# Kernel optimization log

Hardware: AMD Instinct MI355X
Metric: run time of the kernel (lower is better)

The kernel has to match this reference:

```python
import jax, jax.numpy as jnp
import numpy as np

NUM_HEADS = 12
AGENT_NUM = 49

def setup_inputs() -> dict:
    key = jax.random.key(0)
    ks = jax.random.split(key, 5)
    B, N, C = 32, 1176, 768
    x = jax.random.normal(ks[0], (B, N, C), dtype=jnp.float32)
    qkv_w = jax.random.normal(ks[1], (3 * C, C), dtype=jnp.float32) * 0.02
    qkv_b = jax.random.normal(ks[2], (3 * C,), dtype=jnp.float32) * 0.02
    proj_w = jax.random.normal(ks[3], (C, C), dtype=jnp.float32) * 0.02
    proj_b = jax.random.normal(ks[4], (C,), dtype=jnp.float32) * 0.02
    return {"x": x, "qkv_w": qkv_w, "qkv_b": qkv_b, "proj_w": proj_w,
            "proj_b": proj_b, "t_h": 14, "t_w": 14, "s_h": 28, "s_w": 28}

def _softmax_clamped(a):
    # original: float32 clamp to finfo min/max, then softmax(dim=-1)
    fi = jnp.finfo(jnp.float32)
    a = jnp.clip(a.astype(jnp.float32), fi.min, fi.max)
    return jax.nn.softmax(a, axis=-1)

def reference(x, qkv_w, qkv_b, proj_w, proj_b, t_h, t_w, s_h, s_w):
    B, N, C = x.shape
    H = NUM_HEADS
    hd = C // H
    scale = hd ** -0.5
    n_mt = 2 * t_h * t_w
    n_s = s_h * s_w

    qkv = (x @ qkv_w.T + qkv_b).reshape(B, N, 3, H, hd).transpose(2, 0, 3, 1, 4)
    q, k, v = qkv[0], qkv[1], qkv[2]  # [B,H,N,hd]

    q_mt, q_s = q[:, :, :n_mt], q[:, :, n_mt:]
    k_mt = k[:, :, :n_mt]
    v_mt = v[:, :, :n_mt]

    # stage 1: template/memory self-attention
    attn = _softmax_clamped(jnp.einsum('bhqd,bhkd->bhqk', q_mt, k_mt) * scale)
    x_mt = jnp.einsum('bhqk,bhkd->bhqd', attn, v_mt).transpose(0, 2, 1, 3).reshape(B, n_mt, C)

    # agent tokens: pool q_s (replicates original layout-scrambling reshape)
    p = int(AGENT_NUM ** 0.5)  # 7
    agent = q_s.reshape(B, s_h, s_w, C).transpose(0, 3, 1, 2)  # [B,C,s_h,s_w]
    agent = agent.reshape(B, C, p, s_h // p, p, s_w // p).mean(axis=(3, 5))  # exact AdaptiveAvgPool2d(7,7)
    agent = agent.reshape(B, C, AGENT_NUM).transpose(0, 2, 1)  # [B,agent_num,C]
    agent = agent.reshape(B, AGENT_NUM, H, hd).transpose(0, 2, 1, 3)  # [B,H,agent_num,hd]

    # stage 2: agent attends to all keys
    agent_attn = _softmax_clamped(jnp.einsum('bhad,bhkd->bhak', agent * scale, k))
    agent_v = jnp.einsum('bhak,bhkd->bhad', agent_attn, v)  # [B,H,agent_num,hd]

    # stage 3: search queries attend to agent tokens
    q_attn = _softmax_clamped(jnp.einsum('bhqd,bhad->bhqa', q_s * scale, agent))
    x_s = jnp.einsum('bhqa,bhad->bhqd', q_attn, agent_v).transpose(0, 2, 1, 3).reshape(B, n_s, C)

    out = jnp.concatenate([x_mt, x_s], axis=1)
    out = out @ proj_w.T + proj_b
    return out
```

## Files before the change

kernel.cpp:

```cpp
#include <hip/hip_runtime.h>

typedef __attribute__((ext_vector_type(8))) short short8;
typedef __attribute__((ext_vector_type(4))) short short4v;
typedef __attribute__((ext_vector_type(4))) float f32x4;
typedef unsigned short u16;

#define B_    32
#define N_    1176
#define C_    768
#define H_    12
#define HD_   64
#define NMT_  392
#define AG_   49
#define NEGBIG_ (-1.0e4f)

__device__ __forceinline__ u16 f2bf(float f) {
  unsigned u = __float_as_uint(f);
  unsigned r = (u + 0x7fffu + ((u >> 16) & 1u)) >> 16;
  return (u16)r;
}
__device__ __forceinline__ float bf2f(u16 s) {
  return __uint_as_float(((unsigned)s) << 16);
}

__device__ __forceinline__ int xcd_swz(int g, int nwg) {
  const int q = nwg >> 3, r = nwg & 7;
  const int xcd = g & 7, off = g >> 3;
  return (xcd < r ? xcd * (q + 1) : r * (q + 1) + (xcd - r) * q) + off;
}

__global__ __launch_bounds__(256) void split_all(
    const float* __restrict__ x, u16* __restrict__ xbf, int n4x,
    const float* __restrict__ qw, u16* __restrict__ qwh, int n4q,
    const float* __restrict__ pw, u16* __restrict__ pwh,
    u16* __restrict__ pwl, int n4p) {
  const int bid = blockIdx.x;
  const float* in;
  u16 *hi, *lo = nullptr;
  int n4, i0, nblk;
  if (bid < 2048) {
    in = x; hi = xbf; n4 = n4x; i0 = bid; nblk = 2048;
  } else if (bid < 3072) {
    in = qw; hi = qwh; n4 = n4q; i0 = bid - 2048; nblk = 1024;
  } else {
    in = pw; hi = pwh; lo = pwl; n4 = n4p; i0 = bid - 3072; nblk = 512;
  }
  int i = i0 * 256 + threadIdx.x;
  const int stride = nblk * 256;
  const bool dolo = (lo != nullptr);
  for (; i < n4; i += stride) {
    const float4 v = ((const float4*)in)[i];
    const float f[4] = {v.x, v.y, v.z, v.w};
    short4v h, l;
#pragma unroll
    for (int e = 0; e < 4; ++e) {
      u16 hb = f2bf(f[e]);
      h[e] = (short)hb;
      l[e] = (short)f2bf(f[e] - bf2f(hb));
    }
    ((short4v*)hi)[i] = h;
    if (dolo) ((short4v*)lo)[i] = l;
  }
}

__global__ __launch_bounds__(512, 4) void gemm_qkv(
    const u16* __restrict__ A, const u16* __restrict__ Bw,
    const float* __restrict__ bias, u16* __restrict__ qb, u16* __restrict__ kb,
    u16* __restrict__ vb, int Mch) {
  __shared__ u16 SH[24576];
  u16* As = SH;
  u16* Bs = SH + 16384;
  const int tid = threadIdx.x;
  const int swz = xcd_swz(blockIdx.x, gridDim.x);
  const int half = gridDim.x >> 1;
  const int cg = swz / half;
  const int rem = swz - cg * half;
  const int brow = rem / 9;
  const int bcol = cg * 9 + (rem - brow * 9);
  const int m0 = brow * 256, c0 = bcol * 128;
  const int lane = tid & 63, w = tid >> 6;
  const int wr = w >> 1, wc = w & 1;
  const int fr = lane & 15, ko = lane >> 4;
  const int lsw = (lane * 8) ^ (ko << 4);

  f32x4 acc[4][4];
#pragma unroll
  for (int m = 0; m < 4; ++m)
#pragma unroll
    for (int n = 0; n < 4; ++n) acc[m][n] = (f32x4)0.f;

  short8 ra[4], rb[2];
  auto LOADG = [&](int kt) {
#pragma unroll
    for (int i = 0; i < 4; ++i) {
      const int ch = tid + i * 512;
      const int row = ch >> 3, slotk = ch & 7;
      const int ar = min(m0 + row, Mch - 1);
      ra[i] = *(const short8*)&A[(size_t)ar * 768 + kt * 64 + slotk * 8];
    }
#pragma unroll
    for (int i = 0; i < 2; ++i) {
      const int ch = tid + i * 512;
      const int row = ch >> 3, slotk = ch & 7;
      rb[i] = *(const short8*)&Bw[(size_t)(c0 + row) * 768 + kt * 64 + slotk * 8];
    }
  };
  auto WRITE = [&]() {
#pragma unroll
    for (int i = 0; i < 4; ++i) {
      const int ch = tid + i * 512;
      const int row = ch >> 3, slotk = ch & 7;
      const int s = slotk >> 2, sl = slotk & 3;
      const int off = (row >> 4) * 1024 + s * 512 +
                      ((sl * 128 + (row & 15) * 8) ^ (sl << 4));
      *(short8*)&As[off] = ra[i];
    }
#pragma unroll
    for (int i = 0; i < 2; ++i) {
      const int ch = tid + i * 512;
      const int row = ch >> 3, slotk = ch & 7;
      const int s = slotk >> 2, sl = slotk & 3;
      const int off = (row >> 4) * 1024 + s * 512 +
                      ((sl * 128 + (row & 15) * 8) ^ (sl << 4));
      *(short8*)&Bs[off] = rb[i];
    }
  };

  LOADG(0);
  for (int kt = 0; kt < 12; ++kt) {
    __syncthreads();
    WRITE();
    if (kt < 11) LOADG(kt + 1);
    __syncthreads();
#pragma unroll
    for (int s = 0; s < 2; ++s) {
      short8 af[4], bfr[4];
#pragma unroll
      for (int m = 0; m < 4; ++m)
        af[m] = *(const short8*)&As[((wr * 4 + m) * 2 + s) * 512 + lsw];
#pragma unroll
      for (int n = 0; n < 4; ++n)
        bfr[n] = *(const short8*)&Bs[((wc * 4 + n) * 2 + s) * 512 + lsw];
#pragma unroll
      for (int m = 0; m < 4; ++m)
#pragma unroll
        for (int n = 0; n < 4; ++n)
          acc[m][n] = __builtin_amdgcn_mfma_f32_16x16x32_bf16(af[m], bfr[n], acc[m][n], 0, 0, 0);
    }
  }

  const int t = c0 / 768;
  const int hbase = (c0 % 768) >> 6;
#pragma unroll
  for (int p2 = 0; p2 < 2; ++p2) {
    __syncthreads();
    if ((wr >> 1) == p2) {
      const int lbase = (wr & 1) * 64;
      if (t < 2) {
#pragma unroll
        for (int n = 0; n < 4; ++n) {
          const int col = wc * 64 + n * 16 + fr;
          const float bv = bias[c0 + col];
#pragma unroll
          for (int m = 0; m < 4; ++m)
#pragma unroll
            for (int r = 0; r < 4; ++r) {
              const int lrow = lbase + m * 16 + ko * 4 + r;
              SH[lrow * 136 + col] = f2bf(acc[m][n][r] + bv);
            }
        }
      } else {
#pragma unroll
        for (int n = 0; n < 4; ++n) {
          const int col = wc * 64 + n * 16 + fr;
          const float bv = bias[c0 + col];
#pragma unroll
          for (int m = 0; m < 4; ++m)
#pragma unroll
            for (int r = 0; r < 4; ++r) {
              const int lrow = lbase + m * 16 + ko * 4 + r;
              SH[col * 136 + lrow] = f2bf(acc[m][n][r] + bv);
            }
        }
      }
    }
    __syncthreads();
    if (t < 2) {
      u16* dst = (t == 0) ? qb : kb;
#pragma unroll
      for (int it = 0; it < 4; ++it) {
        const int idx = tid + it * 512;
        const int rt = idx >> 4, half2 = (idx >> 3) & 1, p = idx & 7;
        const int mg = m0 + p2 * 128 + rt;
        if (mg < Mch) {
          const int bl = mg / N_, nt = mg - bl * N_;
          const short8 vv = *(const short8*)&SH[rt * 136 + half2 * 64 + p * 8];
          *(short8*)&dst[(((size_t)bl * H_ + hbase + half2) * N_ + nt) * 64 + p * 8] = vv;
        }
      }
    } else {
#pragma unroll
      for (int it = 0; it < 4; ++it) {
        const int idx = tid + it * 512;
        const int ct = idx >> 4, tc = idx & 15;
        const int mg0 = m0 + p2 * 128 + tc * 8;
        if (mg0 < Mch) {
          const int bl = mg0 / N_, nt = mg0 - bl * N_;
          const int d = ct & 63, hh = hbase + (ct >> 6);
          const short8 vv = *(const short8*)&SH[ct * 136 + tc * 8];
          *(short8*)&vb[(((size_t)bl * H_ + hh) * 64 + d) * N_ + nt] = vv;
        }
      }
    }
  }
}

__global__ __launch_bounds__(512, 2) void gemm_proj(
    const u16* __restrict__ Ahg, const u16* __restrict__ Bhg,
    const u16* __restrict__ Blg, const float* __restrict__ bias,
    float* __restrict__ out) {
  __shared__ u16 Ah[16384], Bh[8192], Bl[8192];
  const int tid = threadIdx.x;
  const int swz = xcd_swz(blockIdx.x, gridDim.x);
  const int brow = swz / 6, bcol = swz - brow * 6;
  const int m0 = brow * 256, c0 = bcol * 128;
  const int lane = tid & 63, w = tid >> 6;
  const int wr = w >> 1, wc = w & 1;
  const int fr = lane & 15, ko = lane >> 4;
  const int lsw = (lane * 8) ^ (ko << 4);

  f32x4 acc[4][4];
#pragma unroll
  for (int m = 0; m < 4; ++m)
#pragma unroll
    for (int n = 0; n < 4; ++n) acc[m][n] = (f32x4)0.f;

  short8 ra[4], rbh[2], rbl[2];
  auto LOADG = [&](int kt) {
#pragma unroll
    for (int i = 0; i < 4; ++i) {
      const int ch = tid + i * 512;
      const int row = ch >> 3, slotk = ch & 7;
      ra[i] = *(const short8*)&Ahg[(size_t)(m0 + row) * 768 + kt * 64 + slotk * 8];
    }
#pragma unroll
    for (int i = 0; i < 2; ++i) {
      const int ch = tid + i * 512;
      const int row = ch >> 3, slotk = ch & 7;
      const size_t boff = (size_t)(c0 + row) * 768 + kt * 64 + slotk * 8;
      rbh[i] = *(const short8*)&Bhg[boff];
      rbl[i] = *(const short8*)&Blg[boff];
    }
  };
  auto WRITE = [&]() {
#pragma unroll
    for (int i = 0; i < 4; ++i) {
      const int ch = tid + i * 512;
      const int row = ch >> 3, slotk = ch & 7;
      const int s = slotk >> 2, sl = slotk & 3;
      const int off = (row >> 4) * 1024 + s * 512 +
                      ((sl * 128 + (row & 15) * 8) ^ (sl << 4));
      *(short8*)&Ah[off] = ra[i];
    }
#pragma unroll
    for (int i = 0; i < 2; ++i) {
      const int ch = tid + i * 512;
      const int row = ch >> 3, slotk = ch & 7;
      const int s = slotk >> 2, sl = slotk & 3;
      const int off = (row >> 4) * 1024 + s * 512 +
                      ((sl * 128 + (row & 15) * 8) ^ (sl << 4));
      *(short8*)&Bh[off] = rbh[i];
      *(short8*)&Bl[off] = rbl[i];
    }
  };

  LOADG(0);
  for (int kt = 0; kt < 12; ++kt) {
    __syncthreads();
    WRITE();
    if (kt < 11) LOADG(kt + 1);
    __syncthreads();
#pragma unroll
    for (int s = 0; s < 2; ++s) {
      short8 af[4], bh[4], bl[4];
#pragma unroll
      for (int m = 0; m < 4; ++m)
        af[m] = *(const short8*)&Ah[((wr * 4 + m) * 2 + s) * 512 + lsw];
#pragma unroll
      for (int n = 0; n < 4; ++n) {
        const int off = ((wc * 4 + n) * 2 + s) * 512 + lsw;
        bh[n] = *(const short8*)&Bh[off];
        bl[n] = *(const short8*)&Bl[off];
      }
#pragma unroll
      for (int m = 0; m < 4; ++m)
#pragma unroll
        for (int n = 0; n < 4; ++n) {
          acc[m][n] = __builtin_amdgcn_mfma_f32_16x16x32_bf16(af[m], bh[n], acc[m][n], 0, 0, 0);
          acc[m][n] = __builtin_amdgcn_mfma_f32_16x16x32_bf16(af[m], bl[n], acc[m][n], 0, 0, 0);
        }
    }
  }
#pragma unroll
  for (int n = 0; n < 4; ++n) {
    const int col = c0 + wc * 64 + n * 16 + fr;
    const float bv = bias[col];
#pragma unroll
    for (int m = 0; m < 4; ++m) {
      const int mg = m0 + wr * 64 + m * 16 + ko * 4;
#pragma unroll
      for (int r = 0; r < 4; ++r) out[(size_t)(mg + r) * 768 + col] = acc[m][n][r] + bv;
    }
  }
}

__global__ __launch_bounds__(256) void agent_pool(const u16* __restrict__ q,
                                                  u16* __restrict__ agent) {
  const int wid = threadIdx.x >> 6;
  const int lane = threadIdx.x & 63;
  const int row = blockIdx.x * 4 + wid;
  const int rem = row % (H_ * 64);
  const int b = row / (H_ * 64);
  const int h2 = rem / 64;
  const int a = rem % 64;
  if (a >= AG_) {
    agent[((size_t)b * H_ + h2) * 4096 + a * 64 + lane] = 0;
    return;
  }
  const int ap = a / 7, aq = a % 7;
  float s = 0.f;
#pragma unroll
  for (int i = 0; i < 4; ++i)
#pragma unroll
    for (int j = 0; j < 4; ++j) {
      const int g = (ap * 4 + i) * 336 + (aq * 4 + j) * 12 + h2;
      const int h = g / 784, n = g % 784;
      s += bf2f(q[(((size_t)b * H_ + h) * N_ + NMT_ + n) * HD_ + lane]);
    }
  agent[((size_t)b * H_ + h2) * 4096 + a * 64 + lane] = f2bf(s * 0.0625f);
}

__global__ __launch_bounds__(256, 3) void flash_attn(
    const u16* __restrict__ Q, int q_bh_str, int q_base, int q_row_max, int q_valid,
    const u16* __restrict__ K, int k_bh_str, int k_row_max,
    const u16* __restrict__ Vt, int vt_bh_str, int vt_pitch, int vt_col_max,
    int n_keys, int nkt,
    u16* __restrict__ cch, int b0,
    u16* __restrict__ avT, int mode) {
  __shared__ u16 Qs[4096], Ks[4096], Vts[4096], Ps[4096];
  __shared__ float Ss[64][68];
  __shared__ float mS[64], lS[64], aS[64];

  const int tid = threadIdx.x, bh = blockIdx.x;
  const int q0 = q_base + blockIdx.y * 56;
  const int lane = tid & 63, w = tid >> 6;
  const int fr = lane & 15, ko = lane >> 4;

  const u16* Qb = Q + (size_t)bh * q_bh_str;
  const u16* Kb = K + (size_t)bh * k_bh_str;
  const u16* Vb = Vt + (size_t)bh * vt_bh_str;

#pragma unroll
  for (int i = 0; i < 2; ++i) {
    const int ch = tid + i * 256;
    const int row = ch >> 3, c8 = (ch & 7) << 3;
    const int qr = min(q0 + row, q_row_max);
    const short8 v = *(const short8*)&Qb[(size_t)qr * 64 + c8];
    *(short8*)&Qs[(row * 64 + c8) ^ ((row & 7) << 3)] = v;
  }
  if (tid < 64) { mS[tid] = NEGBIG_; lS[tid] = 0.f; aS[tid] = 0.f; }

  f32x4 oacc[4];
#pragma unroll
  for (int d = 0; d < 4; ++d) oacc[d] = (f32x4)0.f;

  for (int kt = 0; kt < nkt; ++kt) {
#pragma unroll
    for (int i = 0; i < 2; ++i) {
      const int ch = tid + i * 256;
      const int row = ch >> 3, c8 = (ch & 7) << 3;
      const int kr = min(kt * 64 + row, k_row_max);
      const short8 v = *(const short8*)&Kb[(size_t)kr * 64 + c8];
      *(short8*)&Ks[(row * 64 + c8) ^ ((row & 7) << 3)] = v;
    }
#pragma unroll
    for (int i = 0; i < 2; ++i) {
      const int ch = tid + i * 256;
      const int row = ch >> 3, c8 = (ch & 7) << 3;
      const int col8 = kt * 64 + c8;
      const u16* src = &Vb[(size_t)row * vt_pitch];
      short8 v;
      if (col8 + 8 <= vt_col_max) {
        v = *(const short8*)&src[col8];
      } else {
#pragma unroll
        for (int e = 0; e < 8; ++e) v[e] = (short)src[min(col8 + e, vt_col_max - 1)];
      }
      *(short8*)&Vts[(row * 64 + c8) ^ ((row & 7) << 3)] = v;
    }
    __syncthreads();

    short8 aq[2];
#pragma unroll
    for (int s = 0; s < 2; ++s)
      aq[s] = *(const short8*)&Qs[((w * 16 + fr) * 64 + s * 32 + ko * 8) ^ ((fr & 7) << 3)];
#pragma unroll
    for (int j = 0; j < 4; ++j) {
      f32x4 sa = (f32x4)0.f;
#pragma unroll
      for (int s = 0; s < 2; ++s) {
        const short8 bk = *(const short8*)&Ks[((j * 16 + fr) * 64 + s * 32 + ko * 8) ^ ((fr & 7) << 3)];
        sa = __builtin_amdgcn_mfma_f32_16x16x32_bf16(aq[s], bk, sa, 0, 0, 0);
      }
      const int colg = kt * 64 + j * 16 + fr;
      const bool maskc = (colg >= n_keys);
#pragma unroll
      for (int r = 0; r < 4; ++r) {
        const int srow = w * 16 + ko * 4 + r;
        Ss[srow][j * 16 + fr] = maskc ? NEGBIG_ : sa[r] * 0.125f;
      }
    }
    __syncthreads();

    {
      const int r = tid >> 2, jj = tid & 3;
      float sv[16];
      float mx = NEGBIG_;
#pragma unroll
      for (int cc = 0; cc < 4; ++cc) {
        const f32x4 v4 = *(const f32x4*)&Ss[r][jj * 16 + cc * 4];
#pragma unroll
        for (int e = 0; e < 4; ++e) {
          sv[cc * 4 + e] = v4[e];
          mx = fmaxf(mx, v4[e]);
        }
      }
      mx = fmaxf(mx, __shfl_xor(mx, 1));
      mx = fmaxf(mx, __shfl_xor(mx, 2));
      const float mold = mS[r];
      const float mnew = fmaxf(mold, mx);
      float sum = 0.f;
      const int pbase = r * 64 + jj * 16;
      const int px = (r & 7) << 3;
#pragma unroll
      for (int hh = 0; hh < 2; ++hh) {
        short8 ph;
#pragma unroll
        for (int c = 0; c < 8; ++c) {
          const bool mk = (kt * 64 + jj * 16 + hh * 8 + c) >= n_keys;
          const float p = mk ? 0.f : __expf(sv[hh * 8 + c] - mnew);
          sum += p;
          ph[c] = (short)f2bf(p);
        }
        *(short8*)&Ps[(pbase + hh * 8) ^ px] = ph;
      }
      sum += __shfl_xor(sum, 1);
      sum += __shfl_xor(sum, 2);
      if (jj == 0) {
        const float alpha = __expf(mold - mnew);
        aS[r] = alpha;
        lS[r] = lS[r] * alpha + sum;
        mS[r] = mnew;
      }
    }
    __syncthreads();

    float al[4];
#pragma unroll
    for (int r = 0; r < 4; ++r) al[r] = aS[w * 16 + ko * 4 + r];
    short8 ap[2];
#pragma unroll
    for (int s = 0; s < 2; ++s)
      ap[s] = *(const short8*)&Ps[((w * 16 + fr) * 64 + s * 32 + ko * 8) ^ ((fr & 7) << 3)];
#pragma unroll
    for (int dj = 0; dj < 4; ++dj) {
      f32x4 o = oacc[dj];
#pragma unroll
      for (int r = 0; r < 4; ++r) o[r] *= al[r];
#pragma unroll
      for (int s = 0; s < 2; ++s) {
        const short8 bv = *(const short8*)&Vts[((dj * 16 + fr) * 64 + s * 32 + ko * 8) ^ ((fr & 7) << 3)];
        o = __builtin_amdgcn_mfma_f32_16x16x32_bf16(ap[s], bv, o, 0, 0, 0);
      }
      oacc[dj] = o;
    }
    __syncthreads();
  }

  float linv[4];
#pragma unroll
  for (int r = 0; r < 4; ++r) linv[r] = 1.f / fmaxf(lS[w * 16 + ko * 4 + r], 1e-30f);

  if (mode == 0) {
    const int b = bh / H_, h = bh % H_;
#pragma unroll
    for (int dj = 0; dj < 4; ++dj)
#pragma unroll
      for (int r = 0; r < 4; ++r) {
        const int rowl = w * 16 + ko * 4 + r;
        if (rowl < q_valid) {
          const size_t m = (size_t)(b0 + b) * N_ + q0 + rowl;
          cch[m * 768 + h * 64 + dj * 16 + fr] = f2bf(oacc[dj][r] * linv[r]);
        }
      }
  } else {
#pragma unroll
    for (int dj = 0; dj < 4; ++dj)
#pragma unroll
      for (int r = 0; r < 4; ++r) {
        const int a = w * 16 + ko * 4 + r;
        avT[(size_t)bh * 4096 + (dj * 16 + fr) * 64 + a] = f2bf(oacc[dj][r] * linv[r]);
      }
  }
}

__global__ __launch_bounds__(256, 3) void flash_mtqs(
    const u16* __restrict__ qb, const u16* __restrict__ kb,
    const u16* __restrict__ vb, const u16* __restrict__ agent,
    const u16* __restrict__ avT, u16* __restrict__ cch, int b0) {
  __shared__ u16 Qs[4096], Ks[4096], Vts[4096], Ps[4096];
  __shared__ float Ss[64][68];
  __shared__ float mS[64], lS[64], aS[64];

  const int tid = threadIdx.x, bh = blockIdx.x;
  const bool isqs = (blockIdx.y >= 7);
  const int qt = isqs ? (blockIdx.y - 7) : blockIdx.y;
  const int q0 = (isqs ? NMT_ : 0) + qt * 56;
  const int nkt = isqs ? 1 : 7;
  const int n_keys = isqs ? AG_ : NMT_;
  const int vt_pitch = isqs ? 64 : N_;
  const int k_row_max = isqs ? 63 : (N_ - 1);

  const int lane = tid & 63, w = tid >> 6;
  const int fr = lane & 15, ko = lane >> 4;

  const u16* Qb = qb + (size_t)bh * (N_ * HD_);
  const u16* Kb = (isqs ? agent : kb) + (size_t)bh * (isqs ? 4096 : N_ * HD_);
  const u16* Vb = (isqs ? avT : vb) + (size_t)bh * (isqs ? 4096 : N_ * HD_);

#pragma unroll
  for (int i = 0; i < 2; ++i) {
    const int ch = tid + i * 256;
    const int row = ch >> 3, c8 = (ch & 7) << 3;
    const int qr = min(q0 + row, N_ - 1);
    const short8 v = *(const short8*)&Qb[(size_t)qr * 64 + c8];
    *(short8*)&Qs[(row * 64 + c8) ^ ((row & 7) << 3)] = v;
  }
  if (tid < 64) { mS[tid] = NEGBIG_; lS[tid] = 0.f; aS[tid] = 0.f; }

  f32x4 oacc[4];
#pragma unroll
  for (int d = 0; d < 4; ++d) oacc[d] = (f32x4)0.f;

  for (int kt = 0; kt < nkt; ++kt) {
#pragma unroll
    for (int i = 0; i < 2; ++i) {
      const int ch = tid + i * 256;
      const int row = ch >> 3, c8 = (ch & 7) << 3;
      const int kr = min(kt * 64 + row, k_row_max);
      const short8 v = *(const short8*)&Kb[(size_t)kr * 64 + c8];
      *(short8*)&Ks[(row * 64 + c8) ^ ((row & 7) << 3)] = v;
    }
#pragma unroll
    for (int i = 0; i < 2; ++i) {
      const int ch = tid + i * 256;
      const int row = ch >> 3, c8 = (ch & 7) << 3;
      const short8 v = *(const short8*)&Vb[(size_t)row * vt_pitch + kt * 64 + c8];
      *(short8*)&Vts[(row * 64 + c8) ^ ((row & 7) << 3)] = v;
    }
    __syncthreads();

    short8 aq[2];
#pragma unroll
    for (int s = 0; s < 2; ++s)
      aq[s] = *(const short8*)&Qs[((w * 16 + fr) * 64 + s * 32 + ko * 8) ^ ((fr & 7) << 3)];
#pragma unroll
    for (int j = 0; j < 4; ++j) {
      f32x4 sa = (f32x4)0.f;
#pragma unroll
      for (int s = 0; s < 2; ++s) {
        const short8 bk = *(const short8*)&Ks[((j * 16 + fr) * 64 + s * 32 + ko * 8) ^ ((fr & 7) << 3)];
        sa = __builtin_amdgcn_mfma_f32_16x16x32_bf16(aq[s], bk, sa, 0, 0, 0);
      }
      const int colg = kt * 64 + j * 16 + fr;
      const bool maskc = (colg >= n_keys);
#pragma unroll
      for (int r = 0; r < 4; ++r) {
        const int srow = w * 16 + ko * 4 + r;
        Ss[srow][j * 16 + fr] = maskc ? NEGBIG_ : sa[r] * 0.125f;
      }
    }
    __syncthreads();

    {
      const int r = tid >> 2, jj = tid & 3;
      float sv[16];
      float mx = NEGBIG_;
#pragma unroll
      for (int cc = 0; cc < 4; ++cc) {
        const f32x4 v4 = *(const f32x4*)&Ss[r][jj * 16 + cc * 4];
#pragma unroll
        for (int e = 0; e < 4; ++e) {
          sv[cc * 4 + e] = v4[e];
          mx = fmaxf(mx, v4[e]);
        }
      }
      mx = fmaxf(mx, __shfl_xor(mx, 1));
      mx = fmaxf(mx, __shfl_xor(mx, 2));
      const float mold = mS[r];
      const float mnew = fmaxf(mold, mx);
      float sum = 0.f;
      const int pbase = r * 64 + jj * 16;
      const int px = (r & 7) << 3;
#pragma unroll
      for (int hh = 0; hh < 2; ++hh) {
        short8 ph;
#pragma unroll
        for (int c = 0; c < 8; ++c) {
          const bool mk = (kt * 64 + jj * 16 + hh * 8 + c) >= n_keys;
          const float p = mk ? 0.f : __expf(sv[hh * 8 + c] - mnew);
          sum += p;
          ph[c] = (short)f2bf(p);
        }
        *(short8*)&Ps[(pbase + hh * 8) ^ px] = ph;
      }
      sum += __shfl_xor(sum, 1);
      sum += __shfl_xor(sum, 2);
      if (jj == 0) {
        const float alpha = __expf(mold - mnew);
        aS[r] = alpha;
        lS[r] = lS[r] * alpha + sum;
        mS[r] = mnew;
      }
    }
    __syncthreads();

    float al[4];
#pragma unroll
    for (int r = 0; r < 4; ++r) al[r] = aS[w * 16 + ko * 4 + r];
    short8 ap[2];
#pragma unroll
    for (int s = 0; s < 2; ++s)
      ap[s] = *(const short8*)&Ps[((w * 16 + fr) * 64 + s * 32 + ko * 8) ^ ((fr & 7) << 3)];
#pragma unroll
    for (int dj = 0; dj < 4; ++dj) {
      f32x4 o = oacc[dj];
#pragma unroll
      for (int r = 0; r < 4; ++r) o[r] *= al[r];
#pragma unroll
      for (int s = 0; s < 2; ++s) {
        const short8 bv = *(const short8*)&Vts[((dj * 16 + fr) * 64 + s * 32 + ko * 8) ^ ((fr & 7) << 3)];
        o = __builtin_amdgcn_mfma_f32_16x16x32_bf16(ap[s], bv, o, 0, 0, 0);
      }
      oacc[dj] = o;
    }
    __syncthreads();
  }

  float linv[4];
#pragma unroll
  for (int r = 0; r < 4; ++r) linv[r] = 1.f / fmaxf(lS[w * 16 + ko * 4 + r], 1e-30f);

  const int b = bh / H_, h = bh % H_;
#pragma unroll
  for (int dj = 0; dj < 4; ++dj)
#pragma unroll
    for (int r = 0; r < 4; ++r) {
      const int rowl = w * 16 + ko * 4 + r;
      if (rowl < 56) {
        const size_t m = (size_t)(b0 + b) * N_ + q0 + rowl;
        cch[m * 768 + h * 64 + dj * 16 + fr] = f2bf(oacc[dj][r] * linv[r]);
      }
    }
}

extern "C" void kernel_launch(void* const* d_in, const int* in_sizes, int n_in,
                              void* d_out, int out_size, void* d_ws,
                              size_t ws_size, hipStream_t stream) {
  const float* x = (const float*)d_in[0];
  const float* qkv_w = (const float*)d_in[1];
  const float* qkv_b = (const float*)d_in[2];
  const float* proj_w = (const float*)d_in[3];
  const float* proj_b = (const float*)d_in[4];
  float* out = (float*)d_out;
  u16* ws = (u16*)d_ws;

  const size_t XBF = 28901376ull;
  const size_t QW = 2304ull * 768;
  const size_t PW = 768ull * 768;
  const size_t QKV1 = (size_t)H_ * N_ * HD_;
  const size_t AG1 = (size_t)H_ * 64 * 64;

  size_t o = 0;
  u16* xbf = ws + o; o += XBF;
  u16* qwh = ws + o; o += QW;
  u16* pwh = ws + o; o += PW;
  u16* pwl = ws + o; o += PW;
  u16* cch = ws + o; o += XBF;
  const size_t fixed_sh = o;
  const size_t per_sh = 3 * QKV1 + 2 * AG1;

  int cb = 1;
  const int cands[6] = {32, 16, 8, 4, 2, 1};
  for (int i = 0; i < 6; ++i)
    if ((fixed_sh + (size_t)cands[i] * per_sh) * 2 <= ws_size) { cb = cands[i]; break; }

  u16* qb = ws + o; o += cb * QKV1;
  u16* kb = ws + o; o += cb * QKV1;
  u16* vb = ws + o; o += cb * QKV1;
  u16* agent = ws + o; o += cb * AG1;
  u16* avT = ws + o; o += cb * AG1;

  split_all<<<3584, 256, 0, stream>>>(x, xbf, (int)(XBF / 4),
                                      qkv_w, qwh, (int)(QW / 4),
                                      proj_w, pwh, pwl, (int)(PW / 4));

  const int nch = B_ / cb;
  for (int chn = 0; chn < nch; ++chn) {
    const int b0 = chn * cb;
    const int Mch = cb * N_;
    const int nrow = (Mch + 255) / 256;
    gemm_qkv<<<dim3(nrow * 18), 512, 0, stream>>>(
        xbf + (size_t)b0 * N_ * 768, qwh, qkv_b, qb, kb, vb, Mch);
    agent_pool<<<dim3(cb * 192), 256, 0, stream>>>(qb, agent);
    flash_attn<<<dim3(cb * H_, 1), 256, 0, stream>>>(
        agent, 4096, 0, 48, AG_, kb, N_ * HD_, N_ - 1,
        vb, N_ * HD_, N_, N_, N_, 19, nullptr, b0, avT, 1);
    flash_mtqs<<<dim3(cb * H_, 21), 256, 0, stream>>>(
        qb, kb, vb, agent, avT, cch, b0);
  }
  gemm_proj<<<dim3(147 * 6), 512, 0, stream>>>(cch, pwh, pwl, proj_b, out);
}
```

Measured before the change: 450.1 us.

## Split agent attention over key chunks and merge partials in a new kernel

The agent-to-all-keys attention, previously one block per (batch, head) looping over 19 key tiles, is split into 4 key chunks of 5 tiles each. Each chunk writes unnormalized fp32 outputs plus row max and sum to workspace, and a new agent_merge kernel combines them with log-sum-exp weighting into avT. This raises parallelism for a launch that had only cb*12 blocks, at the cost of an extra launch and more workspace traffic. The QKV GEMM block mapping is also simplified to a plain row-major tile order instead of the column-group split.

```diff
diff --git a/kernel.cpp b/kernel.cpp
--- a/kernel.cpp
+++ b/kernel.cpp
@@ -72,11 +72,7 @@
   u16* Bs = SH + 16384;
   const int tid = threadIdx.x;
   const int swz = xcd_swz(blockIdx.x, gridDim.x);
-  const int half = gridDim.x >> 1;
-  const int cg = swz / half;
-  const int rem = swz - cg * half;
-  const int brow = rem / 9;
-  const int bcol = cg * 9 + (rem - brow * 9);
+  const int brow = swz / 18, bcol = swz - brow * 18;
   const int m0 = brow * 256, c0 = bcol * 128;
   const int lane = tid & 63, w = tid >> 6;
   const int wr = w >> 1, wc = w & 1;
@@ -346,13 +342,16 @@
     const u16* __restrict__ Vt, int vt_bh_str, int vt_pitch, int vt_col_max,
     int n_keys, int nkt,
     u16* __restrict__ cch, int b0,
-    u16* __restrict__ avT, int mode) {
+    u16* __restrict__ avT, float* __restrict__ opart,
+    float* __restrict__ mlpart, int BH, int mode) {
   __shared__ u16 Qs[4096], Ks[4096], Vts[4096], Ps[4096];
   __shared__ float Ss[64][68];
   __shared__ float mS[64], lS[64], aS[64];
 
   const int tid = threadIdx.x, bh = blockIdx.x;
-  const int q0 = q_base + blockIdx.y * 56;
+  const int q0 = q_base + (mode == 2 ? 0 : blockIdx.y) * 56;
+  int kt0 = 0, ktend = nkt;
+  if (mode == 2) { kt0 = blockIdx.y * 5; ktend = min(kt0 + 5, nkt); }
   const int lane = tid & 63, w = tid >> 6;
   const int fr = lane & 15, ko = lane >> 4;
 
@@ -374,7 +373,7 @@
 #pragma unroll
   for (int d = 0; d < 4; ++d) oacc[d] = (f32x4)0.f;
 
-  for (int kt = 0; kt < nkt; ++kt) {
+  for (int kt = kt0; kt < ktend; ++kt) {
 #pragma unroll
     for (int i = 0; i < 2; ++i) {
       const int ch = tid + i * 256;
@@ -487,6 +486,24 @@
     __syncthreads();
   }
 
+  if (mode == 2) {
+    const int chunk = blockIdx.y;
+    float* ob = opart + (size_t)(chunk * BH + bh) * 4096;
+#pragma unroll
+    for (int dj = 0; dj < 4; ++dj)
+#pragma unroll
+      for (int r = 0; r < 4; ++r) {
+        const int rowl = w * 16 + ko * 4 + r;
+        ob[rowl * 64 + dj * 16 + fr] = oacc[dj][r];
+      }
+    if (tid < 64) {
+      float* ml = mlpart + ((size_t)(chunk * BH + bh) * 64 + tid) * 2;
+      ml[0] = mS[tid];
+      ml[1] = lS[tid];
+    }
+    return;
+  }
+
   float linv[4];
 #pragma unroll
   for (int r = 0; r < 4; ++r) linv[r] = 1.f / fmaxf(lS[w * 16 + ko * 4 + r], 1e-30f);
@@ -511,6 +528,34 @@
         const int a = w * 16 + ko * 4 + r;
         avT[(size_t)bh * 4096 + (dj * 16 + fr) * 64 + a] = f2bf(oacc[dj][r] * linv[r]);
       }
+  }
+}
+
+__global__ __launch_bounds__(256) void agent_merge(
+    const float* __restrict__ opart, const float* __restrict__ mlpart,
+    u16* __restrict__ avT, int BH) {
+  const int bh = blockIdx.x;
+  const int tid = threadIdx.x;
+  const int d = tid & 63;
+#pragma unroll
+  for (int it = 0; it < 16; ++it) {
+    const int row = (tid >> 6) + it * 4;
+    float mv[4], lv[4], M = NEGBIG_;
+#pragma unroll
+    for (int c = 0; c < 4; ++c) {
+      const float* ml = &mlpart[((size_t)(c * BH + bh) * 64 + row) * 2];
+      mv[c] = ml[0];
+      lv[c] = ml[1];
+      M = fmaxf(M, mv[c]);
+    }
+    float L = 0.f, O = 0.f;
+#pragma unroll
+    for (int c = 0; c < 4; ++c) {
+      const float wgt = __expf(mv[c] - M);
+      L += lv[c] * wgt;
+      O += opart[(size_t)(c * BH + bh) * 4096 + row * 64 + d] * wgt;
+    }
+    avT[(size_t)bh * 4096 + d * 64 + row] = f2bf(O / fmaxf(L, 1e-30f));
   }
 }
 
@@ -690,6 +735,7 @@
   const size_t PW = 768ull * 768;
   const size_t QKV1 = (size_t)H_ * N_ * HD_;
   const size_t AG1 = (size_t)H_ * 64 * 64;
+  const size_t PRT1 = 4ull * H_ * (4096 + 128) * 2;
 
   size_t o = 0;
   u16* xbf = ws + o; o += XBF;
@@ -698,7 +744,7 @@
   u16* pwl = ws + o; o += PW;
   u16* cch = ws + o; o += XBF;
   const size_t fixed_sh = o;
-  const size_t per_sh = 3 * QKV1 + 2 * AG1;
+  const size_t per_sh = 3 * QKV1 + 2 * AG1 + PRT1;
 
   int cb = 1;
   const int cands[6] = {32, 16, 8, 4, 2, 1};
@@ -710,6 +756,8 @@
   u16* vb = ws + o; o += cb * QKV1;
   u16* agent = ws + o; o += cb * AG1;
   u16* avT = ws + o; o += cb * AG1;
+  float* opart = (float*)(ws + o); o += (size_t)4 * cb * H_ * 4096 * 2;
+  float* mlpart = (float*)(ws + o); o += (size_t)4 * cb * H_ * 128 * 2;
 
   split_all<<<3584, 256, 0, stream>>>(x, xbf, (int)(XBF / 4),
                                       qkv_w, qwh, (int)(QW / 4),
@@ -723,9 +771,11 @@
     gemm_qkv<<<dim3(nrow * 18), 512, 0, stream>>>(
         xbf + (size_t)b0 * N_ * 768, qwh, qkv_b, qb, kb, vb, Mch);
     agent_pool<<<dim3(cb * 192), 256, 0, stream>>>(qb, agent);
-    flash_attn<<<dim3(cb * H_, 1), 256, 0, stream>>>(
+    flash_attn<<<dim3(cb * H_, 4), 256, 0, stream>>>(
         agent, 4096, 0, 48, AG_, kb, N_ * HD_, N_ - 1,
-        vb, N_ * HD_, N_, N_, N_, 19, nullptr, b0, avT, 1);
+        vb, N_ * HD_, N_, N_, N_, 19, nullptr, b0, nullptr,
+        opart, mlpart, cb * H_, 2);
+    agent_merge<<<dim3(cb * H_), 256, 0, stream>>>(opart, mlpart, avT, cb * H_);
     flash_mtqs<<<dim3(cb * H_, 21), 256, 0, stream>>>(
         qb, kb, vb, agent, avT, cch, b0);
   }
```

New measurement: 454.2 us. About the same (+0.9%).
